# Kernel optimization log

Measured on AMD Instinct MI355X. Metric: run time of the kernel, lower is better.

## Reference

```python
import math
import jax, jax.numpy as jnp
import numpy as np

B, H, S, D = 2, 16, 2048, 64

def setup_inputs() -> dict:
    key = jax.random.key(0)
    kq, kk, kv = jax.random.split(key, 3)
    return {
        "query": jax.random.normal(kq, (B, H, S, D), dtype=jnp.float32),
        "key": jax.random.normal(kk, (B, H, S, D), dtype=jnp.float32),
        "value": jax.random.normal(kv, (B, H, S, D), dtype=jnp.float32),
        "mask": jnp.ones((B, S, 1), dtype=jnp.float32),  # padding mask, 1 = keep
        "mask_now": 0,  # 0 -> causal (tril diag=0); 1 -> strict causal (diag=-1)
    }

def reference(query, key, value, mask, mask_now):
    d_k = query.shape[-1]
    seq_len = mask.shape[1]
    # [B,H,S,S] scaled scores
    attn_scores = jnp.einsum("bhqd,bhkd->bhqk", query, key) / math.sqrt(d_k)
    diag = -1 if mask_now else 0
    triu_mask = jnp.tril(jnp.ones((seq_len, seq_len), dtype=mask.dtype), diag)  # [S,S]
    # mask[:, :, 0] -> per-query padding mask broadcast over key dim: [B,1,S,S]
    full_mask = triu_mask[None, None, :, :] * mask[:, None, :, 0:1]
    attn_scores = jnp.where(full_mask == 0, jnp.float32(-1e9), attn_scores)
    attn_scores = jax.nn.softmax(attn_scores, axis=-1)
    output = jnp.einsum("bhqk,bhkd->bhqd", attn_scores, value)
    return (output, attn_scores)
```

## Files before the change

### kernel.cpp

```cpp
#include <hip/hip_runtime.h>
#include <math.h>

#define NB 2
#define NH 16
#define SL 2048
#define DD 64
#define QT 64
#define KC 64
#define NCH (SL / KC)
#define NT 256
#define LPS 68

typedef short bf16x8 __attribute__((ext_vector_type(8)));
typedef float f32x4  __attribute__((ext_vector_type(4)));

__device__ __forceinline__ unsigned short f2bf(float x) {
    unsigned u = __float_as_uint(x);
    u += 0x7fffu + ((u >> 16) & 1u);
    return (unsigned short)(u >> 16);
}

__device__ __forceinline__ void lds_barrier() {
    asm volatile("s_waitcnt lgkmcnt(0)\n\ts_barrier" ::: "memory");
}

__global__ __launch_bounds__(256)
void cvt_bf16(const float* __restrict__ in, unsigned short* __restrict__ out, int n4)
{
    int i = blockIdx.x * 256 + threadIdx.x;
    if (i >= n4) return;
    float4 v = ((const float4*)in)[i];
    ushort4 o;
    o.x = f2bf(v.x); o.y = f2bf(v.y); o.z = f2bf(v.z); o.w = f2bf(v.w);
    ((ushort4*)out)[i] = o;
}

__global__ __launch_bounds__(256)
void transpose_v(const float* __restrict__ V, unsigned short* __restrict__ Vt)
{
    __shared__ __align__(16) unsigned short vt[64 * 72];
    const int bh = blockIdx.x >> 5;
    const int s0 = (blockIdx.x & 31) * 64;
    const int t  = threadIdx.x;

    const float4* src = (const float4*)(V + ((size_t)bh * SL + s0) * DD);
    #pragma unroll
    for (int i = 0; i < 4; ++i) {
        int idx = t + i * 256;
        int r = idx >> 4, d4 = idx & 15;
        float4 v = src[r * 16 + d4];
        vt[(d4 * 4 + 0) * 72 + r] = f2bf(v.x);
        vt[(d4 * 4 + 1) * 72 + r] = f2bf(v.y);
        vt[(d4 * 4 + 2) * 72 + r] = f2bf(v.z);
        vt[(d4 * 4 + 3) * 72 + r] = f2bf(v.w);
    }
    __syncthreads();
    const int d = t >> 2, seg = t & 3;
    unsigned short* dst = Vt + ((size_t)bh * DD + d) * SL + s0 + seg * 16;
    uint4 p0 = *(const uint4*)&vt[d * 72 + seg * 16];
    uint4 p1 = *(const uint4*)&vt[d * 72 + seg * 16 + 8];
    *(uint4*)dst = p0;
    *(uint4*)(dst + 8) = p1;
}

__global__ __launch_bounds__(NT, 4)
void attn_mfma(const unsigned short* __restrict__ Qb,
               const unsigned short* __restrict__ Kb,
               const unsigned short* __restrict__ Vt,
               const float* __restrict__ Mg,
               const int* __restrict__ MNg,
               float* __restrict__ Og)
{
    __shared__ __align__(16) float ps[2 * QT * LPS];
    __shared__ int s_deg;

    const int tid  = threadIdx.x;
    const int w    = tid >> 6;
    const int lane = tid & 63;
    const int l15  = lane & 15;
    const int qd   = lane >> 4;

    const int lin  = blockIdx.x;
    const int xcd  = lin & 7;
    const int iloc = lin >> 3;
    const int r    = iloc & 31;
    const int j    = iloc >> 5;
    const int qt   = (j & 1) ? (31 - r) : r;
    const int bh   = xcd * 4 + j;
    const int b    = bh >> 4;
    const int q0   = qt * QT;
    const int rbase = q0 + w * 16;

    const int diag = (MNg[0] != 0) ? -1 : 0;
    if (tid == 0) s_deg = 0;

    int rlim[4]; int anyDeg = 0;
    #pragma unroll
    for (int reg = 0; reg < 4; ++reg) {
        int row = rbase + qd * 4 + reg;
        float m = Mg[(size_t)b * SL + row];
        int rl = row + diag;
        if (m == 0.0f) rl = -1;
        rlim[reg] = rl;
        anyDeg |= (rl < 0);
    }
    __syncthreads();
    if (anyDeg) atomicOr(&s_deg, 1);

    const unsigned short* Qh  = Qb + (size_t)bh * SL * DD;
    const unsigned short* Kh  = Kb + (size_t)bh * SL * DD;
    const unsigned short* Vth = Vt + (size_t)bh * DD * SL;
    float* Oo   = Og + ((size_t)bh * SL + q0) * DD;
    float* Sout = Og + (size_t)NB * NH * SL * DD
                     + (size_t)bh * SL * SL + (size_t)q0 * SL;

    const unsigned short* qrow = Qh + (size_t)(rbase + l15) * DD + qd * 8;
    bf16x8 qf0 = *(const bf16x8*)qrow;
    bf16x8 qf1 = *(const bf16x8*)(qrow + 32);

    __syncthreads();
    const bool blockDeg = (s_deg != 0);
    const int lastA = blockDeg ? (NCH - 1) : qt;

    float lacc[4] = {0.0f, 0.0f, 0.0f, 0.0f};

    bf16x8 ka0[4], ka1[4], kz0[4], kz1[4];
    auto loadK = [&](int kc, bf16x8 (&f0)[4], bf16x8 (&f1)[4]) {
        const int c0 = kc * KC;
        #pragma unroll
        for (int nt = 0; nt < 4; ++nt) {
            const unsigned short* kr = Kh + (size_t)(c0 + nt * 16 + l15) * DD + qd * 8;
            f0[nt] = *(const bf16x8*)kr;
            f1[nt] = *(const bf16x8*)(kr + 32);
        }
    };
    auto stepA = [&](int kc, bf16x8 (&f0)[4], bf16x8 (&f1)[4]) {
        const int c0 = kc * KC;
        #pragma unroll
        for (int nt = 0; nt < 4; ++nt) {
            f32x4 acc = {0.0f, 0.0f, 0.0f, 0.0f};
            __builtin_amdgcn_s_setprio(1);
            acc = __builtin_amdgcn_mfma_f32_16x16x32_bf16(qf0, f0[nt], acc, 0, 0, 0);
            acc = __builtin_amdgcn_mfma_f32_16x16x32_bf16(qf1, f1[nt], acc, 0, 0, 0);
            __builtin_amdgcn_s_setprio(0);
            const int col = c0 + nt * 16 + l15;
            #pragma unroll
            for (int reg = 0; reg < 4; ++reg)
                lacc[reg] += (col <= rlim[reg]) ? __expf(acc[reg] * 0.125f) : 0.0f;
        }
    };

    loadK(0, ka0, ka1);
    for (int kc = 0; kc <= lastA; kc += 2) {
        if (kc + 1 <= lastA) loadK(kc + 1, kz0, kz1);
        stepA(kc, ka0, ka1);
        if (kc + 1 <= lastA) {
            if (kc + 2 <= lastA) loadK(kc + 2, ka0, ka1);
            stepA(kc + 1, kz0, kz1);
        }
    }

    float lsum[4];
    #pragma unroll
    for (int reg = 0; reg < 4; ++reg) {
        float p = lacc[reg];
        p += __shfl_xor(p, 1);  p += __shfl_xor(p, 2);
        p += __shfl_xor(p, 4);  p += __shfl_xor(p, 8);
        lsum[reg] = p;
    }

    float pmul[4], pfill[4];
    #pragma unroll
    for (int reg = 0; reg < 4; ++reg) {
        pmul[reg]  = (rlim[reg] < 0) ? 0.0f : 1.0f / lsum[reg];
        pfill[reg] = (rlim[reg] < 0) ? (1.0f / (float)SL) : 0.0f;
    }

    f32x4 oacc[4];
    #pragma unroll
    for (int nt = 0; nt < 4; ++nt) oacc[nt] = (f32x4){0.0f, 0.0f, 0.0f, 0.0f};

    for (int kc = 0; kc < NCH; ++kc) {
        const int c0 = kc * KC;
        if (kc <= lastA) {
            float* buf = ps + (kc & 1) * (QT * LPS);
            bf16x8 kf0[4], kf1[4];
            #pragma unroll
            for (int nt = 0; nt < 4; ++nt) {
                const unsigned short* kr = Kh + (size_t)(c0 + nt * 16 + l15) * DD + qd * 8;
                kf0[nt] = *(const bf16x8*)kr;
                kf1[nt] = *(const bf16x8*)(kr + 32);
            }
            #pragma unroll
            for (int nt = 0; nt < 4; ++nt) {
                f32x4 acc = {0.0f, 0.0f, 0.0f, 0.0f};
                __builtin_amdgcn_s_setprio(1);
                acc = __builtin_amdgcn_mfma_f32_16x16x32_bf16(qf0, kf0[nt], acc, 0, 0, 0);
                acc = __builtin_amdgcn_mfma_f32_16x16x32_bf16(qf1, kf1[nt], acc, 0, 0, 0);
                __builtin_amdgcn_s_setprio(0);
                const int col = c0 + nt * 16 + l15;
                #pragma unroll
                for (int reg = 0; reg < 4; ++reg) {
                    float val = (col <= rlim[reg]) ? __expf(acc[reg] * 0.125f) * pmul[reg]
                                                   : pfill[reg];
                    buf[(w * 16 + qd * 4 + reg) * LPS + nt * 16 + l15] = val;
                }
            }
            lds_barrier();
            bf16x8 vf0[4], vf1[4];
            #pragma unroll
            for (int nt = 0; nt < 4; ++nt) {
                const unsigned short* vr = Vth + (size_t)(nt * 16 + l15) * SL + c0 + qd * 8;
                vf0[nt] = *(const bf16x8*)vr;
                vf1[nt] = *(const bf16x8*)(vr + 32);
            }
            #pragma unroll
            for (int ii = 0; ii < 4; ++ii) {
                int idx = ii * NT + tid;
                int rr = idx >> 4, c4 = idx & 15;
                *(float4*)(Sout + (size_t)rr * SL + c0 + c4 * 4) =
                    *(const float4*)&buf[rr * LPS + c4 * 4];
            }
            bf16x8 paf[2];
            #pragma unroll
            for (int kb = 0; kb < 2; ++kb) {
                const float* pr = &buf[(w * 16 + l15) * LPS + kb * 32 + qd * 8];
                float4 x = *(const float4*)pr;
                float4 y = *(const float4*)(pr + 4);
                bf16x8 f;
                f[0] = (short)f2bf(x.x); f[1] = (short)f2bf(x.y);
                f[2] = (short)f2bf(x.z); f[3] = (short)f2bf(x.w);
                f[4] = (short)f2bf(y.x); f[5] = (short)f2bf(y.y);
                f[6] = (short)f2bf(y.z); f[7] = (short)f2bf(y.w);
                paf[kb] = f;
            }
            #pragma unroll
            for (int nt = 0; nt < 4; ++nt) {
                __builtin_amdgcn_s_setprio(1);
                oacc[nt] = __builtin_amdgcn_mfma_f32_16x16x32_bf16(paf[0], vf0[nt], oacc[nt], 0, 0, 0);
                oacc[nt] = __builtin_amdgcn_mfma_f32_16x16x32_bf16(paf[1], vf1[nt], oacc[nt], 0, 0, 0);
                __builtin_amdgcn_s_setprio(0);
            }
        } else {
            float4 z = make_float4(0.0f, 0.0f, 0.0f, 0.0f);
            #pragma unroll
            for (int ii = 0; ii < 4; ++ii) {
                int idx = ii * NT + tid;
                int rr = idx >> 4, c4 = idx & 15;
                *(float4*)(Sout + (size_t)rr * SL + c0 + c4 * 4) = z;
            }
        }
    }

    __syncthreads();
    #pragma unroll
    for (int nt = 0; nt < 4; ++nt)
        #pragma unroll
        for (int reg = 0; reg < 4; ++reg)
            ps[(w * 16 + qd * 4 + reg) * LPS + nt * 16 + l15] = oacc[nt][reg];
    __syncthreads();
    #pragma unroll
    for (int ii = 0; ii < 4; ++ii) {
        int idx = ii * NT + tid;
        int rr = idx >> 4, c4 = idx & 15;
        *(float4*)(Oo + (size_t)rr * DD + c4 * 4) = *(const float4*)&ps[rr * LPS + c4 * 4];
    }
}

extern "C" void kernel_launch(void* const* d_in, const int* in_sizes, int n_in,
                              void* d_out, int out_size, void* d_ws, size_t ws_size,
                              hipStream_t stream)
{
    const float* q  = (const float*)d_in[0];
    const float* k  = (const float*)d_in[1];
    const float* v  = (const float*)d_in[2];
    const float* mk = (const float*)d_in[3];
    const int*   mn = (const int*)d_in[4];
    float* out = (float*)d_out;

    const size_t nElem = (size_t)NB * NH * SL * DD;
    unsigned short* Qb = (unsigned short*)d_ws;
    unsigned short* Kp = Qb + nElem;
    unsigned short* Vp = Kp + nElem;

    const int n4 = (int)(nElem / 4);
    cvt_bf16<<<n4 / 256, 256, 0, stream>>>(q, Qb, n4);
    cvt_bf16<<<n4 / 256, 256, 0, stream>>>(k, Kp, n4);
    transpose_v<<<NB * NH * (SL / 64), 256, 0, stream>>>(v, Vp);

    attn_mfma<<<NB * NH * (SL / QT), NT, 0, stream>>>(Qb, Kp, Vp, mk, mn, out);
}
```

Measured before the change: 734.4 us.

## Make waves independent with per-wave row tiles, balanced causal pairing, prescaled Q

Each wave now owns its own 16-row query slab, with rows paired from the front and back of the sequence so that causal work is balanced within a block. Every wave keeps a private LDS slab, so block barriers and the shared degenerate-row flag are gone. Each wave's key range is bounded by its own diagonal rather than the block's, and K/V fragment loads are software-pipelined two at a time to cut register pressure. Q is prescaled by 1/sqrt(d)*log2(e) during conversion so the kernel can use exp2 directly. The trade-off is a slightly different bf16 rounding of Q and less data sharing across waves within a block.

After: 767.1 us. 4.5% more time.

```diff
diff --git a/kernel.cpp b/kernel.cpp
--- a/kernel.cpp
+++ b/kernel.cpp
@@ -5,7 +5,6 @@
 #define NH 16
 #define SL 2048
 #define DD 64
-#define QT 64
 #define KC 64
 #define NCH (SL / KC)
 #define NT 256
@@ -20,18 +19,16 @@
     return (unsigned short)(u >> 16);
 }
 
-__device__ __forceinline__ void lds_barrier() {
-    asm volatile("s_waitcnt lgkmcnt(0)\n\ts_barrier" ::: "memory");
-}
-
 __global__ __launch_bounds__(256)
-void cvt_bf16(const float* __restrict__ in, unsigned short* __restrict__ out, int n4)
+void cvt_bf16(const float* __restrict__ in, unsigned short* __restrict__ out,
+              int n4, float scale)
 {
     int i = blockIdx.x * 256 + threadIdx.x;
     if (i >= n4) return;
     float4 v = ((const float4*)in)[i];
     ushort4 o;
-    o.x = f2bf(v.x); o.y = f2bf(v.y); o.z = f2bf(v.z); o.w = f2bf(v.w);
+    o.x = f2bf(v.x * scale); o.y = f2bf(v.y * scale);
+    o.z = f2bf(v.z * scale); o.w = f2bf(v.w * scale);
     ((ushort4*)out)[i] = o;
 }
 
@@ -71,8 +68,7 @@
                const int* __restrict__ MNg,
                float* __restrict__ Og)
 {
-    __shared__ __align__(16) float ps[2 * QT * LPS];
-    __shared__ int s_deg;
+    __shared__ __align__(16) float ps[4][16 * LPS];
 
     const int tid  = threadIdx.x;
     const int w    = tid >> 6;
@@ -83,187 +79,169 @@
     const int lin  = blockIdx.x;
     const int xcd  = lin & 7;
     const int iloc = lin >> 3;
-    const int r    = iloc & 31;
-    const int j    = iloc >> 5;
-    const int qt   = (j & 1) ? (31 - r) : r;
-    const int bh   = xcd * 4 + j;
+    const int p    = iloc & 31;
+    const int k    = iloc >> 5;
+    const int bh   = xcd * 4 + k;
     const int b    = bh >> 4;
-    const int q0   = qt * QT;
-    const int rbase = q0 + w * 16;
+    const int role = (w + k) & 3;
+    const int r0   = (role < 2) ? (p * 32 + (role & 1) * 16)
+                                : (2016 - p * 32 + (role & 1) * 16);
 
     const int diag = (MNg[0] != 0) ? -1 : 0;
-    if (tid == 0) s_deg = 0;
 
     int rlim[4]; int anyDeg = 0;
     #pragma unroll
     for (int reg = 0; reg < 4; ++reg) {
-        int row = rbase + qd * 4 + reg;
+        int row = r0 + qd * 4 + reg;
         float m = Mg[(size_t)b * SL + row];
         int rl = row + diag;
         if (m == 0.0f) rl = -1;
         rlim[reg] = rl;
         anyDeg |= (rl < 0);
     }
-    __syncthreads();
-    if (anyDeg) atomicOr(&s_deg, 1);
+    const bool waveDeg = __any(anyDeg);
+    const int lastB = waveDeg ? (NCH - 1) : ((r0 + 15 + diag) >> 6);
 
     const unsigned short* Qh  = Qb + (size_t)bh * SL * DD;
     const unsigned short* Kh  = Kb + (size_t)bh * SL * DD;
     const unsigned short* Vth = Vt + (size_t)bh * DD * SL;
-    float* Oo   = Og + ((size_t)bh * SL + q0) * DD;
+    float* Oo   = Og + ((size_t)bh * SL + r0) * DD;
     float* Sout = Og + (size_t)NB * NH * SL * DD
-                     + (size_t)bh * SL * SL + (size_t)q0 * SL;
-
-    const unsigned short* qrow = Qh + (size_t)(rbase + l15) * DD + qd * 8;
+                     + (size_t)bh * SL * SL + (size_t)r0 * SL;
+    float* slab = ps[w];
+
+    const unsigned short* qrow = Qh + (size_t)(r0 + l15) * DD + qd * 8;
     bf16x8 qf0 = *(const bf16x8*)qrow;
     bf16x8 qf1 = *(const bf16x8*)(qrow + 32);
 
-    __syncthreads();
-    const bool blockDeg = (s_deg != 0);
-    const int lastA = blockDeg ? (NCH - 1) : qt;
-
     float lacc[4] = {0.0f, 0.0f, 0.0f, 0.0f};
-
-    bf16x8 ka0[4], ka1[4], kz0[4], kz1[4];
-    auto loadK = [&](int kc, bf16x8 (&f0)[4], bf16x8 (&f1)[4]) {
+    const int total = (lastB + 1) * 4;
+
+    auto ldK = [&](int it, bf16x8& f0, bf16x8& f1) {
+        const unsigned short* kr = Kh + (size_t)(it * 16 + l15) * DD + qd * 8;
+        f0 = *(const bf16x8*)kr;
+        f1 = *(const bf16x8*)(kr + 32);
+    };
+    auto cmpA = [&](int it, bf16x8 f0, bf16x8 f1) {
+        f32x4 acc = {0.0f, 0.0f, 0.0f, 0.0f};
+        __builtin_amdgcn_s_setprio(1);
+        acc = __builtin_amdgcn_mfma_f32_16x16x32_bf16(qf0, f0, acc, 0, 0, 0);
+        acc = __builtin_amdgcn_mfma_f32_16x16x32_bf16(qf1, f1, acc, 0, 0, 0);
+        __builtin_amdgcn_s_setprio(0);
+        const int col = it * 16 + l15;
+        #pragma unroll
+        for (int reg = 0; reg < 4; ++reg)
+            lacc[reg] += (col <= rlim[reg]) ? __builtin_exp2f(acc[reg]) : 0.0f;
+    };
+
+    {
+        bf16x8 A0, A1, B0, B1;
+        ldK(0, A0, A1);
+        for (int it = 0; it < total; it += 2) {
+            if (it + 1 < total) ldK(it + 1, B0, B1);
+            cmpA(it, A0, A1);
+            if (it + 2 < total) ldK(it + 2, A0, A1);
+            if (it + 1 < total) cmpA(it + 1, B0, B1);
+        }
+    }
+
+    float pmul[4], pfill[4];
+    #pragma unroll
+    for (int reg = 0; reg < 4; ++reg) {
+        float s = lacc[reg];
+        s += __shfl_xor(s, 1);  s += __shfl_xor(s, 2);
+        s += __shfl_xor(s, 4);  s += __shfl_xor(s, 8);
+        pmul[reg]  = (rlim[reg] < 0) ? 0.0f : 1.0f / s;
+        pfill[reg] = (rlim[reg] < 0) ? (1.0f / (float)SL) : 0.0f;
+    }
+
+    f32x4 oacc[4];
+    #pragma unroll
+    for (int nt = 0; nt < 4; ++nt) oacc[nt] = (f32x4){0.0f, 0.0f, 0.0f, 0.0f};
+
+    for (int kc = 0; kc <= lastB; ++kc) {
         const int c0 = kc * KC;
+        bf16x8 kb0[2], kb1[2];
+        ldK(kc * 4, kb0[0], kb1[0]);
         #pragma unroll
         for (int nt = 0; nt < 4; ++nt) {
-            const unsigned short* kr = Kh + (size_t)(c0 + nt * 16 + l15) * DD + qd * 8;
-            f0[nt] = *(const bf16x8*)kr;
-            f1[nt] = *(const bf16x8*)(kr + 32);
-        }
-    };
-    auto stepA = [&](int kc, bf16x8 (&f0)[4], bf16x8 (&f1)[4]) {
-        const int c0 = kc * KC;
-        #pragma unroll
-        for (int nt = 0; nt < 4; ++nt) {
+            if (nt < 3) ldK(kc * 4 + nt + 1, kb0[(nt + 1) & 1], kb1[(nt + 1) & 1]);
             f32x4 acc = {0.0f, 0.0f, 0.0f, 0.0f};
             __builtin_amdgcn_s_setprio(1);
-            acc = __builtin_amdgcn_mfma_f32_16x16x32_bf16(qf0, f0[nt], acc, 0, 0, 0);
-            acc = __builtin_amdgcn_mfma_f32_16x16x32_bf16(qf1, f1[nt], acc, 0, 0, 0);
+            acc = __builtin_amdgcn_mfma_f32_16x16x32_bf16(qf0, kb0[nt & 1], acc, 0, 0, 0);
+            acc = __builtin_amdgcn_mfma_f32_16x16x32_bf16(qf1, kb1[nt & 1], acc, 0, 0, 0);
             __builtin_amdgcn_s_setprio(0);
             const int col = c0 + nt * 16 + l15;
             #pragma unroll
-            for (int reg = 0; reg < 4; ++reg)
-                lacc[reg] += (col <= rlim[reg]) ? __expf(acc[reg] * 0.125f) : 0.0f;
-        }
-    };
-
-    loadK(0, ka0, ka1);
-    for (int kc = 0; kc <= lastA; kc += 2) {
-        if (kc + 1 <= lastA) loadK(kc + 1, kz0, kz1);
-        stepA(kc, ka0, ka1);
-        if (kc + 1 <= lastA) {
-            if (kc + 2 <= lastA) loadK(kc + 2, ka0, ka1);
-            stepA(kc + 1, kz0, kz1);
-        }
-    }
-
-    float lsum[4];
-    #pragma unroll
-    for (int reg = 0; reg < 4; ++reg) {
-        float p = lacc[reg];
-        p += __shfl_xor(p, 1);  p += __shfl_xor(p, 2);
-        p += __shfl_xor(p, 4);  p += __shfl_xor(p, 8);
-        lsum[reg] = p;
-    }
-
-    float pmul[4], pfill[4];
-    #pragma unroll
-    for (int reg = 0; reg < 4; ++reg) {
-        pmul[reg]  = (rlim[reg] < 0) ? 0.0f : 1.0f / lsum[reg];
-        pfill[reg] = (rlim[reg] < 0) ? (1.0f / (float)SL) : 0.0f;
-    }
-
-    f32x4 oacc[4];
-    #pragma unroll
-    for (int nt = 0; nt < 4; ++nt) oacc[nt] = (f32x4){0.0f, 0.0f, 0.0f, 0.0f};
-
-    for (int kc = 0; kc < NCH; ++kc) {
-        const int c0 = kc * KC;
-        if (kc <= lastA) {
-            float* buf = ps + (kc & 1) * (QT * LPS);
-            bf16x8 kf0[4], kf1[4];
-            #pragma unroll
-            for (int nt = 0; nt < 4; ++nt) {
-                const unsigned short* kr = Kh + (size_t)(c0 + nt * 16 + l15) * DD + qd * 8;
-                kf0[nt] = *(const bf16x8*)kr;
-                kf1[nt] = *(const bf16x8*)(kr + 32);
+            for (int reg = 0; reg < 4; ++reg) {
+                float val = (col <= rlim[reg]) ? __builtin_exp2f(acc[reg]) * pmul[reg]
+                                               : pfill[reg];
+                slab[(qd * 4 + reg) * LPS + nt * 16 + l15] = val;
             }
-            #pragma unroll
-            for (int nt = 0; nt < 4; ++nt) {
-                f32x4 acc = {0.0f, 0.0f, 0.0f, 0.0f};
-                __builtin_amdgcn_s_setprio(1);
-                acc = __builtin_amdgcn_mfma_f32_16x16x32_bf16(qf0, kf0[nt], acc, 0, 0, 0);
-                acc = __builtin_amdgcn_mfma_f32_16x16x32_bf16(qf1, kf1[nt], acc, 0, 0, 0);
-                __builtin_amdgcn_s_setprio(0);
-                const int col = c0 + nt * 16 + l15;
-                #pragma unroll
-                for (int reg = 0; reg < 4; ++reg) {
-                    float val = (col <= rlim[reg]) ? __expf(acc[reg] * 0.125f) * pmul[reg]
-                                                   : pfill[reg];
-                    buf[(w * 16 + qd * 4 + reg) * LPS + nt * 16 + l15] = val;
-                }
+        }
+        bf16x8 vb0[2], vb1[2];
+        {
+            const unsigned short* vr = Vth + (size_t)l15 * SL + c0 + qd * 8;
+            vb0[0] = *(const bf16x8*)vr;
+            vb1[0] = *(const bf16x8*)(vr + 32);
+        }
+        #pragma unroll
+        for (int ii = 0; ii < 4; ++ii) {
+            int idx = ii * 64 + lane;
+            int rr = idx >> 4, c4 = idx & 15;
+            *(float4*)(Sout + (size_t)rr * SL + c0 + c4 * 4) =
+                *(const float4*)&slab[rr * LPS + c4 * 4];
+        }
+        bf16x8 paf[2];
+        #pragma unroll
+        for (int kb = 0; kb < 2; ++kb) {
+            const float* pr = &slab[l15 * LPS + kb * 32 + qd * 8];
+            float4 x = *(const float4*)pr;
+            float4 y = *(const float4*)(pr + 4);
+            bf16x8 f;
+            f[0] = (short)f2bf(x.x); f[1] = (short)f2bf(x.y);
+            f[2] = (short)f2bf(x.z); f[3] = (short)f2bf(x.w);
+            f[4] = (short)f2bf(y.x); f[5] = (short)f2bf(y.y);
+            f[6] = (short)f2bf(y.z); f[7] = (short)f2bf(y.w);
+            paf[kb] = f;
+        }
+        #pragma unroll
+        for (int nt = 0; nt < 4; ++nt) {
+            if (nt < 3) {
+                const unsigned short* vr = Vth + (size_t)((nt + 1) * 16 + l15) * SL + c0 + qd * 8;
+                vb0[(nt + 1) & 1] = *(const bf16x8*)vr;
+                vb1[(nt + 1) & 1] = *(const bf16x8*)(vr + 32);
             }
-            lds_barrier();
-            bf16x8 vf0[4], vf1[4];
-            #pragma unroll
-            for (int nt = 0; nt < 4; ++nt) {
-                const unsigned short* vr = Vth + (size_t)(nt * 16 + l15) * SL + c0 + qd * 8;
-                vf0[nt] = *(const bf16x8*)vr;
-                vf1[nt] = *(const bf16x8*)(vr + 32);
-            }
+            __builtin_amdgcn_s_setprio(1);
+            oacc[nt] = __builtin_amdgcn_mfma_f32_16x16x32_bf16(paf[0], vb0[nt & 1], oacc[nt], 0, 0, 0);
+            oacc[nt] = __builtin_amdgcn_mfma_f32_16x16x32_bf16(paf[1], vb1[nt & 1], oacc[nt], 0, 0, 0);
+            __builtin_amdgcn_s_setprio(0);
+        }
+    }
+
+    {
+        float4 z = make_float4(0.0f, 0.0f, 0.0f, 0.0f);
+        for (int kc = lastB + 1; kc < NCH; ++kc) {
+            const int c0 = kc * KC;
             #pragma unroll
             for (int ii = 0; ii < 4; ++ii) {
-                int idx = ii * NT + tid;
-                int rr = idx >> 4, c4 = idx & 15;
-                *(float4*)(Sout + (size_t)rr * SL + c0 + c4 * 4) =
-                    *(const float4*)&buf[rr * LPS + c4 * 4];
-            }
-            bf16x8 paf[2];
-            #pragma unroll
-            for (int kb = 0; kb < 2; ++kb) {
-                const float* pr = &buf[(w * 16 + l15) * LPS + kb * 32 + qd * 8];
-                float4 x = *(const float4*)pr;
-                float4 y = *(const float4*)(pr + 4);
-                bf16x8 f;
-                f[0] = (short)f2bf(x.x); f[1] = (short)f2bf(x.y);
-                f[2] = (short)f2bf(x.z); f[3] = (short)f2bf(x.w);
-                f[4] = (short)f2bf(y.x); f[5] = (short)f2bf(y.y);
-                f[6] = (short)f2bf(y.z); f[7] = (short)f2bf(y.w);
-                paf[kb] = f;
-            }
-            #pragma unroll
-            for (int nt = 0; nt < 4; ++nt) {
-                __builtin_amdgcn_s_setprio(1);
-                oacc[nt] = __builtin_amdgcn_mfma_f32_16x16x32_bf16(paf[0], vf0[nt], oacc[nt], 0, 0, 0);
-                oacc[nt] = __builtin_amdgcn_mfma_f32_16x16x32_bf16(paf[1], vf1[nt], oacc[nt], 0, 0, 0);
-                __builtin_amdgcn_s_setprio(0);
-            }
-        } else {
-            float4 z = make_float4(0.0f, 0.0f, 0.0f, 0.0f);
-            #pragma unroll
-            for (int ii = 0; ii < 4; ++ii) {
-                int idx = ii * NT + tid;
+                int idx = ii * 64 + lane;
                 int rr = idx >> 4, c4 = idx & 15;
                 *(float4*)(Sout + (size_t)rr * SL + c0 + c4 * 4) = z;
             }
         }
     }
 
-    __syncthreads();
     #pragma unroll
     for (int nt = 0; nt < 4; ++nt)
         #pragma unroll
         for (int reg = 0; reg < 4; ++reg)
-            ps[(w * 16 + qd * 4 + reg) * LPS + nt * 16 + l15] = oacc[nt][reg];
-    __syncthreads();
+            slab[(qd * 4 + reg) * LPS + nt * 16 + l15] = oacc[nt][reg];
     #pragma unroll
     for (int ii = 0; ii < 4; ++ii) {
-        int idx = ii * NT + tid;
+        int idx = ii * 64 + lane;
         int rr = idx >> 4, c4 = idx & 15;
-        *(float4*)(Oo + (size_t)rr * DD + c4 * 4) = *(const float4*)&ps[rr * LPS + c4 * 4];
+        *(float4*)(Oo + (size_t)rr * DD + c4 * 4) = *(const float4*)&slab[rr * LPS + c4 * 4];
     }
 }
 
@@ -284,9 +262,9 @@
     unsigned short* Vp = Kp + nElem;
 
     const int n4 = (int)(nElem / 4);
-    cvt_bf16<<<n4 / 256, 256, 0, stream>>>(q, Qb, n4);
-    cvt_bf16<<<n4 / 256, 256, 0, stream>>>(k, Kp, n4);
+    cvt_bf16<<<n4 / 256, 256, 0, stream>>>(q, Qb, n4, 0.125f * 1.44269504f);
+    cvt_bf16<<<n4 / 256, 256, 0, stream>>>(k, Kp, n4, 1.0f);
     transpose_v<<<NB * NH * (SL / 64), 256, 0, stream>>>(v, Vp);
 
-    attn_mfma<<<NB * NH * (SL / QT), NT, 0, stream>>>(Qb, Kp, Vp, mk, mn, out);
-}
+    attn_mfma<<<1024, NT, 0, stream>>>(Qb, Kp, Vp, mk, mn, out);
+}
```
